# Kernel optimization log

Hardware: AMD Instinct MI355X
Metric: run time of the kernel (lower is better)

Reference implementation:

```python
import jax, jax.numpy as jnp
import numpy as np

B, S, E, H, L, DFF = 2, 2048, 512, 8, 2, 2048
D = E // H
EPS = 1e-5


def layernorm(x, g, b):
    mu = jnp.mean(x, axis=-1, keepdims=True)
    var = jnp.var(x, axis=-1, keepdims=True)
    return (x - mu) * jax.lax.rsqrt(var + EPS) * g + b


def layernorm_noaffine(x):
    mu = jnp.mean(x, axis=-1, keepdims=True)
    var = jnp.var(x, axis=-1, keepdims=True)
    return (x - mu) * jax.lax.rsqrt(var + EPS)


def setup_inputs() -> dict:
    key = jax.random.key(0)
    ks = jax.random.split(key, 16)
    s = 0.02
    inp = {
        "x": jax.random.normal(ks[0], (B, S, E), dtype=jnp.float32),
        "mask": jax.random.randint(ks[1], (B, S), 0, 2) == 1,
        # per-layer attention projections, stacked over layers
        "wq": jax.random.normal(ks[2], (L, E, E), dtype=jnp.float32) * s,
        "bq": jnp.zeros((L, E), dtype=jnp.float32),
        "wk": jax.random.normal(ks[3], (L, E, E), dtype=jnp.float32) * s,
        "bk": jnp.zeros((L, E), dtype=jnp.float32),
        "wv": jax.random.normal(ks[4], (L, E, E), dtype=jnp.float32) * s,
        "bv": jnp.zeros((L, E), dtype=jnp.float32),
        # shared norms (module defines a single norm1/norm2 used by every layer)
        "g1": jnp.ones((E,), dtype=jnp.float32),
        "b1": jnp.zeros((E,), dtype=jnp.float32),
        "g2": jnp.ones((E,), dtype=jnp.float32),
        "b2": jnp.zeros((E,), dtype=jnp.float32),
        "gf": jnp.ones((E,), dtype=jnp.float32),
        "bf": jnp.zeros((E,), dtype=jnp.float32),
        # shared Dense FFN (single self.dense used after every layer)
        "W1": jax.random.normal(ks[5], (DFF, E), dtype=jnp.float32) * s,
        "B1": jnp.zeros((DFF,), dtype=jnp.float32),
        "W2": jax.random.normal(ks[6], (E, DFF), dtype=jnp.float32) * s,
        "B2": jnp.zeros((E,), dtype=jnp.float32),
    }
    return inp


def _forward(x, wq, bq, wk, bk, wv, bv, g1, b1, g2, b2, gf, bf, W1, B1, W2, B2, mask):
    scale = 1.0 / jnp.sqrt(jnp.float32(D))
    m = mask[:, None, None, :]  # [B,1,1,S] key padding mask, True = pad
    neg_inf = jnp.float32(-jnp.inf)
    for i in range(L):
        h = layernorm(x, g1, b1)  # norm1(x), used for q,k,v
        q = (h @ wq[i].T + bq[i]).reshape(B, S, H, D).transpose(0, 2, 1, 3)
        k = (h @ wk[i].T + bk[i]).reshape(B, S, H, D).transpose(0, 2, 1, 3)
        v = (h @ wv[i].T + bv[i]).reshape(B, S, H, D).transpose(0, 2, 1, 3)
        logits = jnp.einsum("bhqd,bhkd->bhqk", q, k) * scale
        att = jax.nn.softmax(jnp.where(m, neg_inf, logits), axis=-1)
        att = jnp.where(m, 0.0, att)
        out = jnp.einsum("bhqk,bhkd->bhqd", att, v)
        out = out.transpose(0, 2, 1, 3).reshape(B, S, E)
        x = x + layernorm(out, g2, b2)
        # Dense: LayerNorm(no affine) -> Linear -> ReLU -> Linear, residual
        d = layernorm_noaffine(x)
        d = jax.nn.relu(d @ W1.T + B1)
        d = d @ W2.T + B2
        x = x + d
    return layernorm(x, gf, bf)


def reference(x, mask, wq, bq, wk, bk, wv, bv, g1, b1, g2, b2, gf, bf, W1, B1, W2, B2):
    return _forward(x, wq, bq, wk, bk, wv, bv, g1, b1, g2, b2, gf, bf, W1, B1, W2, B2, mask)
```

## Files before the change

### kernel.cpp

```cpp
#include <hip/hip_runtime.h>
#include <hip/hip_bf16.h>

constexpr int BB   = 2;
constexpr int SS   = 2048;
constexpr int EE   = 512;
constexpr int HH   = 8;
constexpr int DD   = 64;
constexpr int DFF_ = 2048;
constexpr int NTOK = BB * SS;
constexpr int NE   = NTOK * EE;
constexpr float EPSF  = 1e-5f;
constexpr float SCL2  = 0.125f * 1.44269504088896f;
constexpr float MBIAS = -1e30f;
constexpr int KSPLIT = 2;
constexpr int KHALF  = SS / KSPLIT;

typedef __bf16 v8bf __attribute__((ext_vector_type(8)));
typedef __bf16 v4bf __attribute__((ext_vector_type(4)));
typedef float  v4f  __attribute__((ext_vector_type(4)));

__device__ __forceinline__ float bf2f(unsigned short u) {
    return __uint_as_float(((unsigned int)u) << 16);
}
__device__ __forceinline__ float bf2f(__bf16 u) {
    unsigned short us = __builtin_bit_cast(unsigned short, u);
    return __uint_as_float(((unsigned int)us) << 16);
}
__device__ __forceinline__ float ldA(const void* p, size_t i, int f) {
    return f ? ((const float*)p)[i] : bf2f(((const unsigned short*)p)[i]);
}
__device__ __forceinline__ void gll16(const void* g, void* l) {
    __builtin_amdgcn_global_load_lds(
        (const __attribute__((address_space(1))) void*)g,
        (__attribute__((address_space(3))) void*)l, 16, 0, 0);
}

__global__ void sniff_kernel(const unsigned short* __restrict__ x, int* flag) {
    __shared__ int cnt[256];
    int t = threadIdx.x, bad = 0;
    for (int i = t; i < 4096; i += 256) {
        float v = bf2f(x[i]);
        if (!(fabsf(v) < 1000.f)) bad++;
    }
    cnt[t] = bad;
    __syncthreads();
    if (t == 0) {
        int s = 0;
        for (int i = 0; i < 256; ++i) s += cnt[i];
        *flag = (s > 8) ? 1 : 0;
    }
}

__global__ __launch_bounds__(256) void cvt_ln(
    const void* __restrict__ in, float* __restrict__ X,
    const void* __restrict__ g, const void* __restrict__ b,
    __bf16* __restrict__ Hb, const int* __restrict__ flagp)
{
    const int f = *flagp;
    const int row = blockIdx.x, t = threadIdx.x;
    const size_t i0 = (size_t)row * EE + t, i1 = i0 + 256;
    float v0 = ldA(in, i0, f);
    float v1 = ldA(in, i1, f);
    float s = v0 + v1, q = v0 * v0 + v1 * v1;
    #pragma unroll
    for (int off = 32; off > 0; off >>= 1) {
        s += __shfl_down(s, off, 64);
        q += __shfl_down(q, off, 64);
    }
    __shared__ float red[8], st[2];
    const int wid = t >> 6;
    if ((t & 63) == 0) { red[wid] = s; red[4 + wid] = q; }
    __syncthreads();
    if (t == 0) {
        float S_ = red[0] + red[1] + red[2] + red[3];
        float Q_ = red[4] + red[5] + red[6] + red[7];
        float mu = S_ / EE;
        st[0] = mu;
        st[1] = rsqrtf(Q_ / EE - mu * mu + EPSF);
    }
    __syncthreads();
    const float mu = st[0], rs = st[1];
    float o0 = (v0 - mu) * rs * ldA(g, t, f)       + ldA(b, t, f);
    float o1 = (v1 - mu) * rs * ldA(g, t + 256, f) + ldA(b, t + 256, f);
    X[i0] = v0; X[i1] = v1;
    Hb[i0] = (__bf16)o0; Hb[i1] = (__bf16)o1;
}

__global__ void wcvt_all(const void* __restrict__ wq, const void* __restrict__ wk,
                         const void* __restrict__ wv, const void* __restrict__ W1,
                         const void* __restrict__ W2, __bf16* __restrict__ out,
                         const int* __restrict__ flagp) {
    const int f = *flagp;
    const int i = (blockIdx.x * blockDim.x + threadIdx.x) * 8;
    constexpr int n1 = 2 * EE * EE;
    constexpr int nf = DFF_ * EE;
    const void* src; int off;
    if      (i < n1)          { src = wq; off = i; }
    else if (i < 2 * n1)      { src = wk; off = i - n1; }
    else if (i < 3 * n1)      { src = wv; off = i - 2 * n1; }
    else if (i < 3 * n1 + nf) { src = W1; off = i - 3 * n1; }
    else                      { src = W2; off = i - 3 * n1 - nf; }
    if (f) {
        const float* p = (const float*)src + off;
        #pragma unroll
        for (int j = 0; j < 8; ++j) out[i + j] = (__bf16)p[j];
    } else {
        *(uint4*)(out + i) = *(const uint4*)((const unsigned short*)src + off);
    }
}

__global__ __launch_bounds__(256) void ln_kernel(
    const float* __restrict__ src,
    const void* __restrict__ g, const void* __restrict__ b,
    __bf16* __restrict__ dstb, void* __restrict__ outp,
    const int* __restrict__ flagp)
{
    const int f = *flagp;
    const int row = blockIdx.x, t = threadIdx.x;
    const float* x = src + (size_t)row * EE;
    float v0 = x[t], v1 = x[t + 256];
    float s = v0 + v1, q = v0 * v0 + v1 * v1;
    #pragma unroll
    for (int off = 32; off > 0; off >>= 1) {
        s += __shfl_down(s, off, 64);
        q += __shfl_down(q, off, 64);
    }
    __shared__ float red[8], st[2];
    const int wid = t >> 6;
    if ((t & 63) == 0) { red[wid] = s; red[4 + wid] = q; }
    __syncthreads();
    if (t == 0) {
        float S_ = red[0] + red[1] + red[2] + red[3];
        float Q_ = red[4] + red[5] + red[6] + red[7];
        float mu = S_ / EE;
        st[0] = mu;
        st[1] = rsqrtf(Q_ / EE - mu * mu + EPSF);
    }
    __syncthreads();
    const float mu = st[0], rs = st[1];
    float o0 = (v0 - mu) * rs, o1 = (v1 - mu) * rs;
    if (g) {
        o0 = o0 * ldA(g, t, f)       + ldA(b, t, f);
        o1 = o1 * ldA(g, t + 256, f) + ldA(b, t + 256, f);
    }
    const size_t i0 = (size_t)row * EE + t, i1 = i0 + 256;
    if (dstb) { dstb[i0] = (__bf16)o0; dstb[i1] = (__bf16)o1; }
    if (outp) {
        if (f) { ((float*)outp)[i0] = o0; ((float*)outp)[i1] = o1; }
        else {
            ((__hip_bfloat16*)outp)[i0] = __float2bfloat16(o0);
            ((__hip_bfloat16*)outp)[i1] = __float2bfloat16(o1);
        }
    }
}

__global__ __launch_bounds__(256) void combine_ln(
    const __bf16* __restrict__ Opart, const float* __restrict__ MLl,
    const void* __restrict__ g2, const void* __restrict__ b2,
    float* __restrict__ X, __bf16* __restrict__ Hb,
    const int* __restrict__ flagp)
{
    const int f = *flagp;
    const int tok = blockIdx.x, t = threadIdx.x;
    const int b = tok >> 11, s_ = tok & 2047;
    __shared__ float cinv[8];
    __shared__ float red[8], st[2];
    if (t < 8) {
        float l = 0.f;
        #pragma unroll
        for (int zz = 0; zz < KSPLIT; ++zz)
            l += MLl[(size_t)(zz * 16 + b * 8 + t) * SS + s_];
        cinv[t] = (l > 0.f) ? 1.f / l : 0.f;
    }
    __syncthreads();
    float a0 = 0.f, a1 = 0.f;
    {
        int c = t, h = c >> 6, d = c & 63;
        #pragma unroll
        for (int zz = 0; zz < KSPLIT; ++zz)
            a0 += bf2f(Opart[((size_t)(zz * 16 + b * 8 + h) * SS + s_) * 64 + d]);
        a0 *= cinv[h];
        c = t + 256; h = c >> 6; d = c & 63;
        #pragma unroll
        for (int zz = 0; zz < KSPLIT; ++zz)
            a1 += bf2f(Opart[((size_t)(zz * 16 + b * 8 + h) * SS + s_) * 64 + d]);
        a1 *= cinv[h];
    }
    const int wid = t >> 6;
    {
        float s = a0 + a1, q = a0 * a0 + a1 * a1;
        #pragma unroll
        for (int off = 32; off > 0; off >>= 1) {
            s += __shfl_down(s, off, 64);
            q += __shfl_down(q, off, 64);
        }
        if ((t & 63) == 0) { red[wid] = s; red[4 + wid] = q; }
    }
    __syncthreads();
    if (t == 0) {
        float S_ = red[0] + red[1] + red[2] + red[3];
        float Q_ = red[4] + red[5] + red[6] + red[7];
        float mu = S_ / EE;
        st[0] = mu;
        st[1] = rsqrtf(Q_ / EE - mu * mu + EPSF);
    }
    __syncthreads();
    const float mu1 = st[0], rs1 = st[1];
    const size_t i0 = (size_t)tok * EE + t, i1 = i0 + 256;
    float l0v = (a0 - mu1) * rs1 * ldA(g2, t, f)       + ldA(b2, t, f);
    float l1v = (a1 - mu1) * rs1 * ldA(g2, t + 256, f) + ldA(b2, t + 256, f);
    float x0 = X[i0] + l0v, x1 = X[i1] + l1v;
    __syncthreads();
    {
        float s = x0 + x1, q = x0 * x0 + x1 * x1;
        #pragma unroll
        for (int off = 32; off > 0; off >>= 1) {
            s += __shfl_down(s, off, 64);
            q += __shfl_down(q, off, 64);
        }
        if ((t & 63) == 0) { red[wid] = s; red[4 + wid] = q; }
    }
    __syncthreads();
    if (t == 0) {
        float S_ = red[0] + red[1] + red[2] + red[3];
        float Q_ = red[4] + red[5] + red[6] + red[7];
        float mu = S_ / EE;
        st[0] = mu;
        st[1] = rsqrtf(Q_ / EE - mu * mu + EPSF);
    }
    __syncthreads();
    const float mu2 = st[0], rs2 = st[1];
    X[i0] = x0; X[i1] = x1;
    Hb[i0] = (__bf16)((x0 - mu2) * rs2);
    Hb[i1] = (__bf16)((x1 - mu2) * rs2);
}

__global__ __launch_bounds__(256) void gemm_mfma(
    const __bf16* __restrict__ A,
    const __bf16* Wa, const __bf16* Wb, const __bf16* Wc,
    const void* ba, const void* bb, const void* bc,
    __bf16* oa, __bf16* ob, __bf16* oc,
    float* __restrict__ Cf,
    int M, int N, int K, int flags,
    size_t welem_off, size_t belem_off, const int* __restrict__ flagp)
{
    const int f = *flagp;
    const int z = blockIdx.z;
    const __bf16* W = (z == 0) ? Wa : (z == 1) ? Wb : Wc;
    const void* bias = (z == 0) ? ba : (z == 1) ? bb : bc;
    __bf16* Cb = (z == 0) ? oa : (z == 1) ? ob : oc;
    W += welem_off;
    int kbeg = 0, kend = K;
    if (flags & 4) {
        const int ks = K >> 2;
        kbeg = z * ks; kend = kbeg + ks;
        if (z != 0) bias = nullptr;
    }

    __shared__ __bf16 As[2][128 * 32];
    __shared__ __bf16 Bs[2][128 * 32];
    const int t = threadIdx.x;
    const int w = t >> 6, lane = t & 63;
    const int quad = lane >> 4, l16 = lane & 15;
    const int wr = w >> 1, wc = w & 1;
    const int bm = blockIdx.x * 128, bn = blockIdx.y * 128;

    v4f acc[4][4] = {};
    const int c0 = t, c1 = t + 256;
    const int r0 = c0 >> 2, e0 = (c0 & 3) * 8;
    const int r1 = c1 >> 2, e1 = (c1 & 3) * 8;

    gll16(A + (size_t)(bm + r0) * K + kbeg + e0, (char*)As[0] + c0 * 16);
    gll16(A + (size_t)(bm + r1) * K + kbeg + e1, (char*)As[0] + c1 * 16);
    gll16(W + (size_t)(bn + r0) * K + kbeg + e0, (char*)Bs[0] + c0 * 16);
    gll16(W + (size_t)(bn + r1) * K + kbeg + e1, (char*)Bs[0] + c1 * 16);

    int p = 0;
    for (int k0 = kbeg; k0 < kend; k0 += 32) {
        __syncthreads();
        if (k0 + 32 < kend) {
            const int kn = k0 + 32, q_ = p ^ 1;
            gll16(A + (size_t)(bm + r0) * K + kn + e0, (char*)As[q_] + c0 * 16);
            gll16(A + (size_t)(bm + r1) * K + kn + e1, (char*)As[q_] + c1 * 16);
            gll16(W + (size_t)(bn + r0) * K + kn + e0, (char*)Bs[q_] + c0 * 16);
            gll16(W + (size_t)(bn + r1) * K + kn + e1, (char*)Bs[q_] + c1 * 16);
        }
        v8bf af[4], bfr[4];
        #pragma unroll
        for (int i = 0; i < 4; ++i) {
            int row = wr * 64 + i * 16 + l16;
            af[i] = *(const v8bf*)&As[p][row * 32 + quad * 8];
        }
        #pragma unroll
        for (int j = 0; j < 4; ++j) {
            int row = wc * 64 + j * 16 + l16;
            bfr[j] = *(const v8bf*)&Bs[p][row * 32 + quad * 8];
        }
        #pragma unroll
        for (int i = 0; i < 4; ++i)
            #pragma unroll
            for (int j = 0; j < 4; ++j)
                acc[i][j] = __builtin_amdgcn_mfma_f32_16x16x32_bf16(
                    af[i], bfr[j], acc[i][j], 0, 0, 0);
        p ^= 1;
    }

    float bvv[4];
    #pragma unroll
    for (int j = 0; j < 4; ++j) {
        int col = bn + wc * 64 + j * 16 + l16;
        bvv[j] = bias ? ldA(bias, belem_off + col, f) : 0.f;
    }

    if ((flags & 8) && z == 2) {
        #pragma unroll
        for (int i = 0; i < 4; ++i) {
            const int row0 = bm + wr * 64 + i * 16 + quad * 4;
            const int b_ = row0 >> 11, sl = row0 & 2047;
            const int s64 = sl & ~63, sloc = sl & 63;
            const int slot = (sloc & 32) + ((sloc >> 2) & 3) * 8 + ((sloc >> 4) & 1) * 4;
            #pragma unroll
            for (int j = 0; j < 4; ++j) {
                const int col = bn + wc * 64 + j * 16 + l16;
                const int h_ = col >> 6, d_ = col & 63;
                v4bf u;
                #pragma unroll
                for (int r = 0; r < 4; ++r) u[r] = (__bf16)(acc[i][j][r] + bvv[j]);
                *(v4bf*)(Cb + ((size_t)((b_ * 8 + h_) * 64 + d_)) * SS + s64 + slot) = u;
            }
        }
        return;
    }

    #pragma unroll
    for (int i = 0; i < 4; ++i) {
        const int rowb = bm + wr * 64 + i * 16 + quad * 4;
        #pragma unroll
        for (int j = 0; j < 4; ++j) {
            const int col = bn + wc * 64 + j * 16 + l16;
            #pragma unroll
            for (int r = 0; r < 4; ++r) {
                float v = acc[i][j][r] + bvv[j];
                if (flags & 1) v = fmaxf(v, 0.f);
                const size_t idx = (size_t)(rowb + r) * N + col;
                if (flags & 4)      unsafeAtomicAdd(&Cf[idx], v);
                else if (flags & 2) Cf[idx] += v;
                else                Cb[idx] = (__bf16)v;
            }
        }
    }
}

__global__ __launch_bounds__(256) void attn_mfma(
    const __bf16* __restrict__ Qg, const __bf16* __restrict__ Kg,
    const __bf16* __restrict__ Vtg, const int* __restrict__ mask,
    __bf16* __restrict__ Opart, float* __restrict__ MLl)
{
    __shared__ __bf16 Ks[64][72];
    __shared__ __bf16 Vs[64][72];
    __shared__ float  mkf[64];

    const int t = threadIdx.x;
    const int w = t >> 6, lane = t & 63;
    const int quad = lane >> 4, l16 = lane & 15;
    const int bh = blockIdx.y, b = bh >> 3, hh = bh & 7;
    const int q0 = blockIdx.x * 128;
    const int z  = blockIdx.z;
    const int kof = z * KHALF;

    const __bf16* qrow0 = Qg + ((size_t)(b * SS + q0 + w * 32 + l16)) * EE + hh * DD + quad * 8;
    const __bf16* qrow1 = qrow0 + (size_t)16 * EE;
    const v8bf qa00 = *(const v8bf*)qrow0;
    const v8bf qa01 = *(const v8bf*)(qrow0 + 32);
    const v8bf qa10 = *(const v8bf*)qrow1;
    const v8bf qa11 = *(const v8bf*)(qrow1 + 32);

    const int lr = t >> 2, lc = (t & 3) * 16;
    const __bf16* kbase = Kg  + ((size_t)(b * SS + kof + lr)) * EE + hh * DD + lc;
    const __bf16* vbase = Vtg + ((size_t)((b * 8 + hh) * 64 + lr)) * SS + kof + lc;

    v8bf ka0 = *(const v8bf*)kbase, ka1 = *(const v8bf*)(kbase + 8);
    v8bf va0 = *(const v8bf*)vbase, va1 = *(const v8bf*)(vbase + 8);
    float mb = 0.f;
    if (t < 64) mb = mask[b * SS + kof + t] ? MBIAS : 0.f;

    float l0 = 0.f, l1 = 0.f;
    v4f o0[4] = {}, o1[4] = {};

    #pragma unroll 1
    for (int k0 = 0; k0 < KHALF; k0 += 64) {
        *(v8bf*)&Ks[lr][lc]     = ka0;
        *(v8bf*)&Ks[lr][lc + 8] = ka1;
        *(v8bf*)&Vs[lr][lc]     = va0;
        *(v8bf*)&Vs[lr][lc + 8] = va1;
        if (t < 64) mkf[t] = mb;
        __syncthreads();
        if (k0 + 64 < KHALF) {
            ka0 = *(const v8bf*)(kbase + (size_t)(k0 + 64) * EE);
            ka1 = *(const v8bf*)(kbase + (size_t)(k0 + 64) * EE + 8);
            va0 = *(const v8bf*)(vbase + (k0 + 64));
            va1 = *(const v8bf*)(vbase + (k0 + 64) + 8);
            if (t < 64) mb = mask[b * SS + kof + k0 + 64 + t] ? MBIAS : 0.f;
        }

        v4f s0[4], s1[4];
        __builtin_amdgcn_s_setprio(1);
        #pragma unroll
        for (int j = 0; j < 4; ++j) {
            v8bf kf0 = *(const v8bf*)&Ks[j * 16 + l16][quad * 8];
            v8bf kf1 = *(const v8bf*)&Ks[j * 16 + l16][32 + quad * 8];
            v4f za = {}, zb = {};
            za = __builtin_amdgcn_mfma_f32_16x16x32_bf16(kf0, qa00, za, 0, 0, 0);
            za = __builtin_amdgcn_mfma_f32_16x16x32_bf16(kf1, qa01, za, 0, 0, 0);
            zb = __builtin_amdgcn_mfma_f32_16x16x32_bf16(kf0, qa10, zb, 0, 0, 0);
            zb = __builtin_amdgcn_mfma_f32_16x16x32_bf16(kf1, qa11, zb, 0, 0, 0);
            s0[j] = za; s1[j] = zb;
        }
        __builtin_amdgcn_s_setprio(0);
        float4 mk4[4];
        #pragma unroll
        for (int j = 0; j < 4; ++j) mk4[j] = *(const float4*)&mkf[j * 16 + quad * 4];

        v8bf p00, p01, p10, p11;
        float t0 = 0.f, t1 = 0.f;
        #pragma unroll
        for (int j = 0; j < 4; ++j) {
            float a0 = exp2f(fmaf(s0[j][0], SCL2, mk4[j].x));
            float a1 = exp2f(fmaf(s0[j][1], SCL2, mk4[j].y));
            float a2 = exp2f(fmaf(s0[j][2], SCL2, mk4[j].z));
            float a3 = exp2f(fmaf(s0[j][3], SCL2, mk4[j].w));
            float b0 = exp2f(fmaf(s1[j][0], SCL2, mk4[j].x));
            float b1 = exp2f(fmaf(s1[j][1], SCL2, mk4[j].y));
            float b2 = exp2f(fmaf(s1[j][2], SCL2, mk4[j].z));
            float b3 = exp2f(fmaf(s1[j][3], SCL2, mk4[j].w));
            t0 += (a0 + a1) + (a2 + a3);
            t1 += (b0 + b1) + (b2 + b3);
            if (j < 2) {
                p00[j * 4 + 0] = (__bf16)a0; p00[j * 4 + 1] = (__bf16)a1;
                p00[j * 4 + 2] = (__bf16)a2; p00[j * 4 + 3] = (__bf16)a3;
                p10[j * 4 + 0] = (__bf16)b0; p10[j * 4 + 1] = (__bf16)b1;
                p10[j * 4 + 2] = (__bf16)b2; p10[j * 4 + 3] = (__bf16)b3;
            } else {
                p01[(j - 2) * 4 + 0] = (__bf16)a0; p01[(j - 2) * 4 + 1] = (__bf16)a1;
                p01[(j - 2) * 4 + 2] = (__bf16)a2; p01[(j - 2) * 4 + 3] = (__bf16)a3;
                p11[(j - 2) * 4 + 0] = (__bf16)b0; p11[(j - 2) * 4 + 1] = (__bf16)b1;
                p11[(j - 2) * 4 + 2] = (__bf16)b2; p11[(j - 2) * 4 + 3] = (__bf16)b3;
            }
        }
        l0 += t0; l1 += t1;

        __builtin_amdgcn_s_setprio(1);
        #pragma unroll
        for (int dt = 0; dt < 4; ++dt) {
            v8bf vf0 = *(const v8bf*)&Vs[dt * 16 + l16][quad * 8];
            v8bf vf1 = *(const v8bf*)&Vs[dt * 16 + l16][32 + quad * 8];
            o0[dt] = __builtin_amdgcn_mfma_f32_16x16x32_bf16(vf0, p00, o0[dt], 0, 0, 0);
            o0[dt] = __builtin_amdgcn_mfma_f32_16x16x32_bf16(vf1, p01, o0[dt], 0, 0, 0);
            o1[dt] = __builtin_amdgcn_mfma_f32_16x16x32_bf16(vf0, p10, o1[dt], 0, 0, 0);
            o1[dt] = __builtin_amdgcn_mfma_f32_16x16x32_bf16(vf1, p11, o1[dt], 0, 0, 0);
        }
        __builtin_amdgcn_s_setprio(0);
        __syncthreads();
    }

    l0 += __shfl_xor(l0, 16, 64);
    l0 += __shfl_xor(l0, 32, 64);
    l1 += __shfl_xor(l1, 16, 64);
    l1 += __shfl_xor(l1, 32, 64);

    const size_t qi0 = (size_t)(z * 16 + bh) * SS + (q0 + w * 32 + l16);
    const size_t qi1 = qi0 + 16;
    __bf16* op0 = Opart + qi0 * 64;
    __bf16* op1 = Opart + qi1 * 64;
    #pragma unroll
    for (int dt = 0; dt < 4; ++dt) {
        v4bf u0, u1;
        #pragma unroll
        for (int r = 0; r < 4; ++r) { u0[r] = (__bf16)o0[dt][r]; u1[r] = (__bf16)o1[dt][r]; }
        *(v4bf*)(op0 + dt * 16 + quad * 4) = u0;
        *(v4bf*)(op1 + dt * 16 + quad * 4) = u1;
    }
    if (quad == 0) { MLl[qi0] = l0; MLl[qi1] = l1; }
}

extern "C" void kernel_launch(void* const* d_in, const int* in_sizes, int n_in,
                              void* d_out, int out_size, void* d_ws, size_t ws_size,
                              hipStream_t stream) {
    const void* x_in = d_in[0];
    const int*  mask = (const int*)d_in[1];
    const void* wq = d_in[2];  const void* bq = d_in[3];
    const void* wk = d_in[4];  const void* bk = d_in[5];
    const void* wv = d_in[6];  const void* bv = d_in[7];
    const void* g1 = d_in[8];  const void* b1 = d_in[9];
    const void* g2 = d_in[10]; const void* b2 = d_in[11];
    const void* gf = d_in[12]; const void* bfp= d_in[13];
    const void* W1 = d_in[14]; const void* B1 = d_in[15];
    const void* W2 = d_in[16]; const void* B2 = d_in[17];

    float* base = (float*)d_ws;
    int*   flag = (int*)base;
    float* X   = base + 16;
    float* fQ  = X + NE;
    float* fK  = fQ + NE / 2;
    float* fV  = fK + NE / 2;
    float* fH  = fV + NE / 2;
    float* fW  = fH + NE / 2;
    __bf16* Qb    = (__bf16*)fQ;
    __bf16* Kb    = (__bf16*)fK;
    __bf16* Vtg   = (__bf16*)fV;
    __bf16* Hb    = (__bf16*)fH;
    __bf16* wqc = (__bf16*)fW;
    __bf16* wkc = wqc + 2 * EE * EE;
    __bf16* wvc = wkc + 2 * EE * EE;
    __bf16* W1c = wvc + 2 * EE * EE;
    __bf16* W2c = W1c + DFF_ * EE;
    float* MLl = (float*)(W2c + (size_t)EE * DFF_);
    float* fO  = MLl + (size_t)KSPLIT * 16 * SS;
    __bf16* Opart = (__bf16*)fO;
    __bf16* MID   = (__bf16*)fO;

    sniff_kernel<<<1, 256, 0, stream>>>((const unsigned short*)x_in, flag);
    cvt_ln<<<NTOK, 256, 0, stream>>>(x_in, X, g1, b1, Hb, flag);
    wcvt_all<<<1792, 256, 0, stream>>>(wq, wk, wv, W1, W2, wqc, flag);

    const dim3 gQKV(NTOK / 128, EE / 128, 3);
    const dim3 gF1 (NTOK / 128, DFF_ / 128, 1);
    const dim3 gF2 (NTOK / 128, EE / 128, 4);
    const dim3 gAtt(SS / 128, BB * HH, KSPLIT);

    for (int l = 0; l < 2; ++l) {
        const size_t wo = (size_t)l * EE * EE, bo = (size_t)l * EE;
        if (l > 0)
            ln_kernel<<<NTOK, 256, 0, stream>>>(X, g1, b1, Hb, nullptr, flag);
        gemm_mfma<<<gQKV, 256, 0, stream>>>(Hb, wqc, wkc, wvc, bq, bk, bv,
            Qb, Kb, Vtg, nullptr, NTOK, EE, EE, 8, wo, bo, flag);
        attn_mfma<<<gAtt, 256, 0, stream>>>(Qb, Kb, Vtg, mask, Opart, MLl);
        combine_ln<<<NTOK, 256, 0, stream>>>(Opart, MLl, g2, b2, X, Hb, flag);
        gemm_mfma<<<gF1, 256, 0, stream>>>(Hb, W1c, W1c, W1c, B1, B1, B1,
            MID, MID, MID, nullptr, NTOK, DFF_, EE, 1, 0, 0, flag);
        gemm_mfma<<<gF2, 256, 0, stream>>>(MID, W2c, W2c, W2c, B2, B2, B2,
            nullptr, nullptr, nullptr, X, NTOK, EE, DFF_, 2 | 4, 0, 0, flag);
    }
    ln_kernel<<<NTOK, 256, 0, stream>>>(X, gf, bfp, nullptr, d_out, flag);
}
```

Baseline: 365.7 us.

## Double GEMM K-tile to 64 and XOR-swizzle LDS layout

```diff
diff --git a/kernel.cpp b/kernel.cpp
--- a/kernel.cpp
+++ b/kernel.cpp
@@ -257,8 +257,8 @@
         if (z != 0) bias = nullptr;
     }
 
-    __shared__ __bf16 As[2][128 * 32];
-    __shared__ __bf16 Bs[2][128 * 32];
+    __shared__ __bf16 As[2][128 * 64];
+    __shared__ __bf16 Bs[2][128 * 64];
     const int t = threadIdx.x;
     const int w = t >> 6, lane = t & 63;
     const int quad = lane >> 4, l16 = lane & 15;
@@ -266,44 +266,53 @@
     const int bm = blockIdx.x * 128, bn = blockIdx.y * 128;
 
     v4f acc[4][4] = {};
-    const int c0 = t, c1 = t + 256;
-    const int r0 = c0 >> 2, e0 = (c0 & 3) * 8;
-    const int r1 = c1 >> 2, e1 = (c1 & 3) * 8;
-
-    gll16(A + (size_t)(bm + r0) * K + kbeg + e0, (char*)As[0] + c0 * 16);
-    gll16(A + (size_t)(bm + r1) * K + kbeg + e1, (char*)As[0] + c1 * 16);
-    gll16(W + (size_t)(bn + r0) * K + kbeg + e0, (char*)Bs[0] + c0 * 16);
-    gll16(W + (size_t)(bn + r1) * K + kbeg + e1, (char*)Bs[0] + c1 * 16);
+
+    #define STAGE_TILE(dst, src, rowbase, kk)                                   \
+        _Pragma("unroll")                                                       \
+        for (int ii = 0; ii < 4; ++ii) {                                        \
+            const int c  = t + 256 * ii;                                        \
+            const int r  = c >> 3, cc = c & 7;                                  \
+            const int es = ((cc ^ (r & 7)) * 8);                                \
+            gll16(src + (size_t)(rowbase + r) * K + kk + es,                    \
+                  (char*)(dst) + c * 16);                                       \
+        }
+
+    STAGE_TILE(As[0], A, bm, kbeg)
+    STAGE_TILE(Bs[0], W, bn, kbeg)
 
     int p = 0;
-    for (int k0 = kbeg; k0 < kend; k0 += 32) {
+    for (int k0 = kbeg; k0 < kend; k0 += 64) {
         __syncthreads();
-        if (k0 + 32 < kend) {
-            const int kn = k0 + 32, q_ = p ^ 1;
-            gll16(A + (size_t)(bm + r0) * K + kn + e0, (char*)As[q_] + c0 * 16);
-            gll16(A + (size_t)(bm + r1) * K + kn + e1, (char*)As[q_] + c1 * 16);
-            gll16(W + (size_t)(bn + r0) * K + kn + e0, (char*)Bs[q_] + c0 * 16);
-            gll16(W + (size_t)(bn + r1) * K + kn + e1, (char*)Bs[q_] + c1 * 16);
-        }
-        v8bf af[4], bfr[4];
-        #pragma unroll
-        for (int i = 0; i < 4; ++i) {
-            int row = wr * 64 + i * 16 + l16;
-            af[i] = *(const v8bf*)&As[p][row * 32 + quad * 8];
-        }
-        #pragma unroll
-        for (int j = 0; j < 4; ++j) {
-            int row = wc * 64 + j * 16 + l16;
-            bfr[j] = *(const v8bf*)&Bs[p][row * 32 + quad * 8];
-        }
-        #pragma unroll
-        for (int i = 0; i < 4; ++i)
+        if (k0 + 64 < kend) {
+            const int kn = k0 + 64, q_ = p ^ 1;
+            STAGE_TILE(As[q_], A, bm, kn)
+            STAGE_TILE(Bs[q_], W, bn, kn)
+        }
+        #pragma unroll
+        for (int ks = 0; ks < 2; ++ks) {
+            v8bf af[4], bfr[4];
             #pragma unroll
-            for (int j = 0; j < 4; ++j)
-                acc[i][j] = __builtin_amdgcn_mfma_f32_16x16x32_bf16(
-                    af[i], bfr[j], acc[i][j], 0, 0, 0);
+            for (int i = 0; i < 4; ++i) {
+                const int row = wr * 64 + i * 16 + l16;
+                const int ph  = (quad + ks * 4) ^ (row & 7);
+                af[i] = *(const v8bf*)&As[p][row * 64 + ph * 8];
+            }
+            #pragma unroll
+            for (int j = 0; j < 4; ++j) {
+                const int row = wc * 64 + j * 16 + l16;
+                const int ph  = (quad + ks * 4) ^ (row & 7);
+                bfr[j] = *(const v8bf*)&Bs[p][row * 64 + ph * 8];
+            }
+            #pragma unroll
+            for (int i = 0; i < 4; ++i)
+                #pragma unroll
+                for (int j = 0; j < 4; ++j)
+                    acc[i][j] = __builtin_amdgcn_mfma_f32_16x16x32_bf16(
+                        af[i], bfr[j], acc[i][j], 0, 0, 0);
+        }
         p ^= 1;
     }
+    #undef STAGE_TILE
 
     float bvv[4];
     #pragma unroll
```

Result: no change. 358.9 us (-1.9%).
